# Optimization experiments

Hardware: AMD Instinct MI355X
Metric: run time of the kernel (lower is better)

Reference implementation:

```python
import jax, jax.numpy as jnp
import numpy as np

B, T, C = 4, 2048, 1024
H = 16
D = C // H  # head_dim = 64


def setup_inputs() -> dict:
    key = jax.random.key(0)
    k1, k2, k3 = jax.random.split(key, 3)
    x = jax.random.normal(k1, (B, T, C), dtype=jnp.float32)
    # torch Linear weights are [out_features, in_features]; scale like default init
    W_qkv = jax.random.normal(k2, (3 * C, C), dtype=jnp.float32) * (1.0 / np.sqrt(C))
    W_proj = jax.random.normal(k3, (C, C), dtype=jnp.float32) * (1.0 / np.sqrt(C))
    return {"x": x, "W_qkv": W_qkv, "W_proj": W_proj}


def reference(x, W_qkv, W_proj):
    # qkv projection: x @ W_qkv.T -> (B,T,3C), split into q,k,v
    qkv = jnp.einsum('btc,oc->bto', x, W_qkv)
    q, k, v = jnp.split(qkv, 3, axis=-1)
    # reshape to (B,H,T,D)
    q = q.reshape(B, T, H, D).transpose(0, 2, 1, 3)
    k = k.reshape(B, T, H, D).transpose(0, 2, 1, 3)
    v = v.reshape(B, T, H, D).transpose(0, 2, 1, 3)
    scale = jnp.sqrt(jnp.float32(D))
    # explicit (B,H,T,T) scores, as in the original module
    attn = jnp.einsum('bhqd,bhkd->bhqk', q, k) / scale
    causal = jnp.tril(jnp.ones((T, T), dtype=bool))
    attn = jnp.where(causal, attn, -jnp.inf)
    attn = jax.nn.softmax(attn, axis=-1)
    out = jnp.einsum('bhqk,bhkd->bhqd', attn, v)
    out = out.transpose(0, 2, 1, 3).reshape(B, T, C)
    return jnp.einsum('btc,oc->bto', out, W_proj)
```

## Files before the change

### kernel.cpp

```cpp
#include <hip/hip_runtime.h>

typedef __attribute__((ext_vector_type(8))) short short8;
typedef __attribute__((ext_vector_type(4))) float f32x4;
typedef __attribute__((ext_vector_type(16))) float f32x16;
typedef __attribute__((ext_vector_type(4))) unsigned int u32x4;

#define AS1(p) ((const __attribute__((address_space(1))) void*)(p))
#define AS3(p) ((__attribute__((address_space(3))) void*)(p))

#define B_ 4
#define T_ 2048
#define C_ 1024
#define H_ 16
#define D_ 64
#define M_ (B_*T_)

#define MFIX 16.0f

__device__ __forceinline__ unsigned short f2bf(float f) {
  union { float f; unsigned u; } v; v.f = f;
  return (unsigned short)((v.u + 0x7fffu + ((v.u >> 16) & 1u)) >> 16);
}

__device__ __forceinline__ unsigned cvt_pk_bf16(float lo, float hi2) {
  unsigned r;
  asm("v_cvt_pk_bf16_f32 %0, %1, %2" : "=v"(r) : "v"(lo), "v"(hi2));
  return r;
}

__device__ __forceinline__ float exp2_fast(float x) {
  return __builtin_amdgcn_exp2f(x);
}

__global__ void cast_f32_bf16(const float* __restrict__ in, unsigned short* __restrict__ out, int n) {
  int i = (blockIdx.x * blockDim.x + threadIdx.x) * 4;
  int stride = gridDim.x * blockDim.x * 4;
  for (; i < n; i += stride) {
    float4 f = *reinterpret_cast<const float4*>(in + i);
    ushort4 o;
    o.x = f2bf(f.x); o.y = f2bf(f.y); o.z = f2bf(f.z); o.w = f2bf(f.w);
    *reinterpret_cast<ushort4*>(out + i) = o;
  }
}

template<int EPI>
__global__ __launch_bounds__(256) void gemm_bt(
    const unsigned short* __restrict__ A, const unsigned short* __restrict__ Bt,
    float* __restrict__ Cout, int M, int N, int K,
    unsigned short* __restrict__ qb, unsigned short* __restrict__ kb,
    unsigned short* __restrict__ vtb) {
  __shared__ unsigned short As[2][128 * 32];
  __shared__ unsigned short Bs[2][128 * 32];
  const int tid = threadIdx.x;
  const int lane = tid & 63;
  const int w = tid >> 6;
  const int wr = w >> 1, wc = w & 1;
  const int lr = lane & 15, lg = lane >> 4;
  const int ntiles = N >> 7;
  const int nwg = gridDim.x;
  const int cpx = nwg >> 3;
  const int wg = (blockIdx.x & 7) * cpx + (blockIdx.x >> 3);
  const int mt = wg / ntiles, nt = wg % ntiles;
  const int m0 = mt << 7, n0 = nt << 7;

  f32x4 acc[4][4];
  #pragma unroll
  for (int i = 0; i < 4; i++)
    #pragma unroll
    for (int j = 0; j < 4; j++) acc[i][j] = (f32x4){0.f, 0.f, 0.f, 0.f};

  const int wbase = tid & ~63;

  auto stage = [&](int buf, int k0) {
    #pragma unroll
    for (int t = 0; t < 2; t++) {
      int slot = t * 256 + tid;
      int row = slot >> 2, kg = slot & 3;
      const unsigned short* ga = A + (size_t)(m0 + row) * K + k0 + kg * 8;
      char* la = (char*)As[buf] + (size_t)(t * 256 + wbase) * 16;
      __builtin_amdgcn_global_load_lds(AS1(ga), AS3(la), 16, 0, 0);
      const unsigned short* gb = Bt + (size_t)(n0 + row) * K + k0 + kg * 8;
      char* lb = (char*)Bs[buf] + (size_t)(t * 256 + wbase) * 16;
      __builtin_amdgcn_global_load_lds(AS1(gb), AS3(lb), 16, 0, 0);
    }
  };

  const int nIter = K >> 5;
  stage(0, 0);

  for (int it = 0; it < nIter; ++it) {
    const int cur = it & 1;
    if (it + 1 < nIter) {
      stage(cur ^ 1, (it + 1) << 5);
      asm volatile("s_waitcnt vmcnt(4)" ::: "memory");
    } else {
      asm volatile("s_waitcnt vmcnt(0)" ::: "memory");
    }
    __builtin_amdgcn_sched_barrier(0);
    __builtin_amdgcn_s_barrier();
    __builtin_amdgcn_sched_barrier(0);

    short8 af[4], bf[4];
    #pragma unroll
    for (int i = 0; i < 4; i++) {
      af[i] = *reinterpret_cast<const short8*>(&As[cur][(wr * 64 + i * 16 + lr) * 32 + lg * 8]);
      bf[i] = *reinterpret_cast<const short8*>(&Bs[cur][(wc * 64 + i * 16 + lr) * 32 + lg * 8]);
    }
    #pragma unroll
    for (int i = 0; i < 4; i++)
      #pragma unroll
      for (int j = 0; j < 4; j++)
        acc[i][j] = __builtin_amdgcn_mfma_f32_16x16x32_bf16(af[i], bf[j], acc[i][j], 0, 0, 0);

    __builtin_amdgcn_sched_barrier(0);
    __builtin_amdgcn_s_barrier();
  }

  #pragma unroll
  for (int i = 0; i < 4; i++) {
    #pragma unroll
    for (int j = 0; j < 4; j++) {
      #pragma unroll
      for (int r = 0; r < 4; r++) {
        int row = m0 + wr * 64 + i * 16 + lg * 4 + r;
        int col = n0 + wc * 64 + j * 16 + lr;
        float v = acc[i][j][r];
        if (EPI == 0) {
          Cout[(size_t)row * N + col] = v;
        } else {
          int which = col >> 10;
          int c = col & 1023;
          int h = c >> 6, d = c & 63;
          int b = row >> 11, t2 = row & 2047;
          if (which == 0) {
            qb[(((size_t)(b * H_ + h)) * T_ + t2) * D_ + d] = f2bf(v * 0.18033688f);
          } else if (which == 1) {
            kb[(((size_t)(b * H_ + h)) * T_ + t2) * D_ + d] = f2bf(v);
          } else {
            vtb[(((size_t)(b * H_ + h)) * D_ + d) * T_ + t2] = f2bf(v);
          }
        }
      }
    }
  }
}

__global__ __launch_bounds__(128, 2) void attn_fwd(
    const unsigned short* __restrict__ qb, const unsigned short* __restrict__ kb,
    const unsigned short* __restrict__ vtb, unsigned short* __restrict__ ob) {
  __shared__ unsigned short Kl[2 * 64 * 64];
  const int tid = threadIdx.x;
  const int lane = tid & 63;
  const int w = tid >> 6;
  const int q31 = lane & 31;
  const int hi = lane >> 5;

  const int bid = blockIdx.x;
  const int bh = (bid & 7) * 8 + ((bid >> 3) & 7);
  const int qt = 15 - (bid >> 6);
  const int qb0 = qt << 7;
  const int b = bh >> 4, h = bh & 15;

  const unsigned short* Q  = qb  + (size_t)bh * T_ * D_;
  const unsigned short* Kp = kb  + (size_t)bh * T_ * D_;
  const unsigned short* Vt = vtb + (size_t)bh * D_ * T_;

  const int qloA = qb0 + w * 64;
  const int qloB = qloA + 32;
  const int qgA = qloA + q31;
  const int qgB = qloB + q31;

  short8 qfA[4], qfB[4];
  #pragma unroll
  for (int ch = 0; ch < 4; ch++) {
    qfA[ch] = *reinterpret_cast<const short8*>(Q + qgA * D_ + ch * 16 + hi * 8);
    qfB[ch] = *reinterpret_cast<const short8*>(Q + qgB * D_ + ch * 16 + hi * 8);
  }

  f32x16 accA0, accA1, accB0, accB1;
  #pragma unroll
  for (int r = 0; r < 16; r++) { accA0[r] = 0.f; accA1[r] = 0.f; accB0[r] = 0.f; accB1[r] = 0.f; }
  float lA = 0.f, lB = 0.f;

  auto stage = [&](int buf, int k0) {
    #pragma unroll
    for (int sh = 0; sh < 4; sh++) {
      int s = sh * 128 + tid;
      int row = s >> 3;
      int xlin = (s & 7) * 16;
      int src = xlin ^ ((row & 7) << 4);
      const unsigned short* g = Kp + (k0 + row) * D_ + (src >> 1);
      char* l = (char*)Kl + buf * 8192 + (size_t)(sh * 128 + (tid & ~63)) * 16;
      __builtin_amdgcn_global_load_lds(AS1(g), AS3(l), 16, 0, 0);
    }
  };

  const int nt = qb0 / 64 + 2;
  stage(0, 0);
  __syncthreads();

  for (int t = 0; t < nt; t++) {
    const int k0 = t * 64;
    if (t + 1 < nt) stage((t + 1) & 1, k0 + 64);

    if (k0 <= qloA + 63) {
      short8 vf[2][4];
      #pragma unroll
      for (int ds = 0; ds < 2; ds++)
        #pragma unroll
        for (int kk = 0; kk < 4; kk++)
          vf[ds][kk] = *reinterpret_cast<const short8*>(
              Vt + (ds * 32 + q31) * T_ + k0 + kk * 16 + hi * 8);
      __builtin_amdgcn_sched_barrier(0);

      const char* kbase = (const char*)Kl + (t & 1) * 8192;

      f32x16 sA0, sA1, sB0, sB1;
      #pragma unroll
      for (int r = 0; r < 16; r++) { sA0[r] = 0.f; sA1[r] = 0.f; sB0[r] = 0.f; sB1[r] = 0.f; }
      __builtin_amdgcn_s_setprio(1);
      #pragma unroll
      for (int kc = 0; kc < 2; kc++) {
        const int row = kc * 32 + q31;
        const int sw = (row & 7) << 4;
        #pragma unroll
        for (int ch = 0; ch < 4; ch++) {
          short8 kf = *reinterpret_cast<const short8*>(kbase + row * 128 + ((ch * 32 + hi * 16) ^ sw));
          if (kc == 0) {
            sA0 = __builtin_amdgcn_mfma_f32_32x32x16_bf16(kf, qfA[ch], sA0, 0, 0, 0);
            sB0 = __builtin_amdgcn_mfma_f32_32x32x16_bf16(kf, qfB[ch], sB0, 0, 0, 0);
          } else {
            sA1 = __builtin_amdgcn_mfma_f32_32x32x16_bf16(kf, qfA[ch], sA1, 0, 0, 0);
            sB1 = __builtin_amdgcn_mfma_f32_32x32x16_bf16(kf, qfB[ch], sB1, 0, 0, 0);
          }
        }
      }
      __builtin_amdgcn_s_setprio(0);

      if (k0 + 63 > qloA) {
        #pragma unroll
        for (int r = 0; r < 16; r++) {
          const int kl = (r & 3) + 8 * (r >> 2) + 4 * hi;
          if (k0 + kl > qgA)      sA0[r] = -INFINITY;
          if (k0 + 32 + kl > qgA) sA1[r] = -INFINITY;
        }
      }
      if (k0 + 63 > qloB) {
        #pragma unroll
        for (int r = 0; r < 16; r++) {
          const int kl = (r & 3) + 8 * (r >> 2) + 4 * hi;
          if (k0 + kl > qgB)      sB0[r] = -INFINITY;
          if (k0 + 32 + kl > qgB) sB1[r] = -INFINITY;
        }
      }

      #pragma unroll
      for (int r = 0; r < 16; r++) {
        sA0[r] = exp2_fast(sA0[r] - MFIX); sA1[r] = exp2_fast(sA1[r] - MFIX);
        sB0[r] = exp2_fast(sB0[r] - MFIX); sB1[r] = exp2_fast(sB1[r] - MFIX);
      }
      {
        float tsA[8], tsB[8];
        #pragma unroll
        for (int r = 0; r < 8; r++) {
          tsA[r] = (sA0[r] + sA0[r + 8]) + (sA1[r] + sA1[r + 8]);
          tsB[r] = (sB0[r] + sB0[r + 8]) + (sB1[r] + sB1[r + 8]);
        }
        #pragma unroll
        for (int off = 4; off > 0; off >>= 1)
          #pragma unroll
          for (int r = 0; r < off; r++) { tsA[r] += tsA[r + off]; tsB[r] += tsB[r + off]; }
        lA += tsA[0];
        lB += tsB[0];
      }

      #pragma unroll
      for (int kc = 0; kc < 2; kc++) {
        unsigned w8A[8], rw8A[8], w8B[8], rw8B[8];
        #pragma unroll
        for (int j = 0; j < 8; j++) {
          float aA  = (kc == 0) ? sA0[2 * j] : sA1[2 * j];
          float bA  = (kc == 0) ? sA0[2 * j + 1] : sA1[2 * j + 1];
          w8A[j] = cvt_pk_bf16(aA, bA);
          float aB  = (kc == 0) ? sB0[2 * j] : sB1[2 * j];
          float bB  = (kc == 0) ? sB0[2 * j + 1] : sB1[2 * j + 1];
          w8B[j] = cvt_pk_bf16(aB, bB);
        }
        #pragma unroll
        for (int j = 0; j < 8; j++) {
          rw8A[j] = (unsigned)__shfl_xor((int)w8A[j], 32);
          rw8B[j] = (unsigned)__shfl_xor((int)w8B[j], 32);
        }

        __builtin_amdgcn_s_setprio(1);
        #pragma unroll
        for (int ks = 0; ks < 2; ks++) {
          unsigned a0 = hi ? rw8A[4 * ks + 2] : w8A[4 * ks + 0];
          unsigned a1 = hi ? rw8A[4 * ks + 3] : w8A[4 * ks + 1];
          unsigned a2 = hi ? w8A[4 * ks + 2]  : rw8A[4 * ks + 0];
          unsigned a3 = hi ? w8A[4 * ks + 3]  : rw8A[4 * ks + 1];
          u32x4 pwA = {a0, a1, a2, a3};
          unsigned b0 = hi ? rw8B[4 * ks + 2] : w8B[4 * ks + 0];
          unsigned b1 = hi ? rw8B[4 * ks + 3] : w8B[4 * ks + 1];
          unsigned b2 = hi ? w8B[4 * ks + 2]  : rw8B[4 * ks + 0];
          unsigned b3 = hi ? w8B[4 * ks + 3]  : rw8B[4 * ks + 1];
          u32x4 pwB = {b0, b1, b2, b3};
          union { u32x4 u; short8 s; } cvA, cvB;
          cvA.u = pwA; cvB.u = pwB;
          const int kk = kc * 2 + ks;
          #pragma unroll
          for (int ds = 0; ds < 2; ds++) {
            if (ds == 0) {
              accA0 = __builtin_amdgcn_mfma_f32_32x32x16_bf16(vf[0][kk], cvA.s, accA0, 0, 0, 0);
              accB0 = __builtin_amdgcn_mfma_f32_32x32x16_bf16(vf[0][kk], cvB.s, accB0, 0, 0, 0);
            } else {
              accA1 = __builtin_amdgcn_mfma_f32_32x32x16_bf16(vf[1][kk], cvA.s, accA1, 0, 0, 0);
              accB1 = __builtin_amdgcn_mfma_f32_32x32x16_bf16(vf[1][kk], cvB.s, accB1, 0, 0, 0);
            }
          }
        }
        __builtin_amdgcn_s_setprio(0);
      }
    }
    __syncthreads();
  }

  lA += __shfl_xor(lA, 32);
  lB += __shfl_xor(lB, 32);

  {
    const float invA = 1.f / lA;
    unsigned short* orow = ob + ((size_t)(b * T_ + qgA)) * C_ + h * D_;
    #pragma unroll
    for (int ds = 0; ds < 2; ds++) {
      #pragma unroll
      for (int g = 0; g < 4; g++) {
        ushort4 o4;
        if (ds == 0) {
          o4.x = f2bf(accA0[4 * g + 0] * invA); o4.y = f2bf(accA0[4 * g + 1] * invA);
          o4.z = f2bf(accA0[4 * g + 2] * invA); o4.w = f2bf(accA0[4 * g + 3] * invA);
        } else {
          o4.x = f2bf(accA1[4 * g + 0] * invA); o4.y = f2bf(accA1[4 * g + 1] * invA);
          o4.z = f2bf(accA1[4 * g + 2] * invA); o4.w = f2bf(accA1[4 * g + 3] * invA);
        }
        *reinterpret_cast<ushort4*>(orow + ds * 32 + 8 * g + 4 * hi) = o4;
      }
    }
  }
  {
    const float invB = 1.f / lB;
    unsigned short* orow = ob + ((size_t)(b * T_ + qgB)) * C_ + h * D_;
    #pragma unroll
    for (int ds = 0; ds < 2; ds++) {
      #pragma unroll
      for (int g = 0; g < 4; g++) {
        ushort4 o4;
        if (ds == 0) {
          o4.x = f2bf(accB0[4 * g + 0] * invB); o4.y = f2bf(accB0[4 * g + 1] * invB);
          o4.z = f2bf(accB0[4 * g + 2] * invB); o4.w = f2bf(accB0[4 * g + 3] * invB);
        } else {
          o4.x = f2bf(accB1[4 * g + 0] * invB); o4.y = f2bf(accB1[4 * g + 1] * invB);
          o4.z = f2bf(accB1[4 * g + 2] * invB); o4.w = f2bf(accB1[4 * g + 3] * invB);
        }
        *reinterpret_cast<ushort4*>(orow + ds * 32 + 8 * g + 4 * hi) = o4;
      }
    }
  }
}

extern "C" void kernel_launch(void* const* d_in, const int* in_sizes, int n_in,
                              void* d_out, int out_size, void* d_ws, size_t ws_size,
                              hipStream_t stream) {
  const float* x = (const float*)d_in[0];
  const float* W_qkv = (const float*)d_in[1];
  const float* W_proj = (const float*)d_in[2];
  float* out = (float*)d_out;

  char* ws = (char*)d_ws;
  unsigned short* xb     = (unsigned short*)(ws);
  unsigned short* wqkvb  = (unsigned short*)(ws + 16777216);
  unsigned short* wprojb = (unsigned short*)(ws + 23068672);
  unsigned short* qb     = (unsigned short*)(ws + 25165824);
  unsigned short* kb     = (unsigned short*)(ws + 41943040);
  unsigned short* vtb    = (unsigned short*)(ws + 58720256);
  unsigned short* ob     = xb;

  const int nx = M_ * C_;
  const int nwqkv = 3 * C_ * C_;
  const int nwproj = C_ * C_;

  cast_f32_bf16<<<2048, 256, 0, stream>>>(x, xb, nx);
  cast_f32_bf16<<<2048, 256, 0, stream>>>(W_qkv, wqkvb, nwqkv);
  cast_f32_bf16<<<1024, 256, 0, stream>>>(W_proj, wprojb, nwproj);

  gemm_bt<1><<<(M_ / 128) * (3 * C_ / 128), 256, 0, stream>>>(
      xb, wqkvb, nullptr, M_, 3 * C_, C_, qb, kb, vtb);

  attn_fwd<<<B_ * H_ * (T_ / 128), 128, 0, stream>>>(qb, kb, vtb, ob);

  gemm_bt<0><<<(M_ / 128) * (C_ / 128), 256, 0, stream>>>(
      ob, wprojb, out, M_, C_, C_, nullptr, nullptr, nullptr);
}
```

Baseline: 211.9 us.

## Add 256x256 swizzled-LDS QKV GEMM kernel and simplify projection GEMM sync

Replaces the 128x128 templated GEMM used for the QKV projection with a dedicated 512-thread kernel. It uses 256x256 output tiles, 64-wide K tiles, XOR-swizzled LDS staging, and a four-phase loop that issues the next tile's loads between MFMA groups, with raised wave priority during MFMAs. The goal is more data reuse per LDS load and fewer bank conflicts. The cost is 128 KB of LDS per block and a grid of only 384 blocks, which may leave CUs poorly balanced. The output-projection GEMM loses its template and now uses plain __syncthreads instead of hand-placed vmcnt waits and barriers.

```diff
diff --git a/kernel.cpp b/kernel.cpp
--- a/kernel.cpp
+++ b/kernel.cpp
@@ -43,12 +43,133 @@
   }
 }
 
-template<int EPI>
+__global__ __launch_bounds__(512, 2) void gemm256_qkv(
+    const unsigned short* __restrict__ A, const unsigned short* __restrict__ Bt,
+    int M, int N, int K,
+    unsigned short* __restrict__ qb, unsigned short* __restrict__ kb,
+    unsigned short* __restrict__ vtb) {
+  __shared__ unsigned short Ls[2][2][2][128 * 64];
+  const int tid = threadIdx.x;
+  const int lane = tid & 63;
+  const int wid = tid >> 6;
+  const int wm = wid >> 2;
+  const int wn = wid & 3;
+  const int lr = lane & 15, lg = lane >> 4;
+  const int ntb_cnt = N >> 8;
+  const int nwg = gridDim.x;
+  const int cpx = nwg >> 3;
+  const int wg = (blockIdx.x & 7) * cpx + (blockIdx.x >> 3);
+  const int mt = wg / ntb_cnt, ntb = wg % ntb_cnt;
+  const int m0 = mt << 8, n0 = ntb << 8;
+
+  f32x4 acc[8][4];
+  #pragma unroll
+  for (int i = 0; i < 8; i++)
+    #pragma unroll
+    for (int j = 0; j < 4; j++) acc[i][j] = (f32x4){0.f, 0.f, 0.f, 0.f};
+
+  const int wbase16 = (tid & ~63) * 16;
+
+  auto stage = [&](int buf, int mat, int half, int k0) {
+    const unsigned short* srcbase = (mat == 0) ? (A  + (size_t)(m0 + half * 128) * K)
+                                               : (Bt + (size_t)(n0 + half * 128) * K);
+    char* ldsbase = (char*)&Ls[buf][mat][half][0];
+    #pragma unroll
+    for (int i = 0; i < 2; i++) {
+      int s = i * 512 + tid;
+      int row = s >> 3;
+      int src = ((s & 7) * 16) ^ ((row & 7) << 4);
+      const unsigned short* g = srcbase + (size_t)row * K + k0 + (src >> 1);
+      char* l = ldsbase + i * 8192 + wbase16;
+      __builtin_amdgcn_global_load_lds(AS1(g), AS3(l), 16, 0, 0);
+    }
+  };
+
+  const int ktiles = K >> 6;
+  stage(0, 0, 0, 0); stage(0, 0, 1, 0); stage(0, 1, 0, 0); stage(0, 1, 1, 0);
+
+  for (int t = 0; t < ktiles; ++t) {
+    const int cur = t & 1;
+    const int nk0 = (t + 1) << 6;
+    const bool more = (t + 1 < ktiles);
+    short8 bfrag[4][2];
+
+    #pragma unroll
+    for (int p = 0; p < 4; p++) {
+      if (more) stage(cur ^ 1, p >> 1, p & 1, nk0);
+      if (p == 0) {
+        if (more) asm volatile("s_waitcnt vmcnt(2)" ::: "memory");
+        else      asm volatile("s_waitcnt vmcnt(0)" ::: "memory");
+      }
+      __builtin_amdgcn_sched_barrier(0);
+      __builtin_amdgcn_s_barrier();
+      __builtin_amdgcn_sched_barrier(0);
+
+      if (p == 0) {
+        #pragma unroll
+        for (int ni = 0; ni < 4; ni++)
+          #pragma unroll
+          for (int ks = 0; ks < 2; ks++) {
+            const int rih = (wn & 1) * 64 + ni * 16 + lr;
+            bfrag[ni][ks] = *reinterpret_cast<const short8*>(
+                (const char*)&Ls[cur][1][wn >> 1][0] + rih * 128 +
+                ((ks * 64 + lg * 16) ^ ((lr & 7) << 4)));
+          }
+      }
+      short8 af[2][2];
+      #pragma unroll
+      for (int m2 = 0; m2 < 2; m2++)
+        #pragma unroll
+        for (int ks = 0; ks < 2; ks++) {
+          const int rih = (2 * p + m2) * 16 + lr;
+          af[m2][ks] = *reinterpret_cast<const short8*>(
+              (const char*)&Ls[cur][0][wm][0] + rih * 128 +
+              ((ks * 64 + lg * 16) ^ ((lr & 7) << 4)));
+        }
+
+      __builtin_amdgcn_s_setprio(1);
+      #pragma unroll
+      for (int m2 = 0; m2 < 2; m2++)
+        #pragma unroll
+        for (int ni = 0; ni < 4; ni++)
+          #pragma unroll
+          for (int ks = 0; ks < 2; ks++)
+            acc[2 * p + m2][ni] = __builtin_amdgcn_mfma_f32_16x16x32_bf16(
+                af[m2][ks], bfrag[ni][ks], acc[2 * p + m2][ni], 0, 0, 0);
+      __builtin_amdgcn_s_setprio(0);
+      __builtin_amdgcn_sched_barrier(0);
+      __builtin_amdgcn_s_barrier();
+    }
+  }
+
+  #pragma unroll
+  for (int mi = 0; mi < 8; mi++) {
+    #pragma unroll
+    for (int ni = 0; ni < 4; ni++) {
+      #pragma unroll
+      for (int r = 0; r < 4; r++) {
+        int row = m0 + wm * 128 + mi * 16 + lg * 4 + r;
+        int col = n0 + wn * 64 + ni * 16 + lr;
+        float v = acc[mi][ni][r];
+        int which = col >> 10;
+        int c = col & 1023;
+        int h = c >> 6, d = c & 63;
+        int b = row >> 11, t2 = row & 2047;
+        if (which == 0) {
+          qb[(((size_t)(b * H_ + h)) * T_ + t2) * D_ + d] = f2bf(v * 0.18033688f);
+        } else if (which == 1) {
+          kb[(((size_t)(b * H_ + h)) * T_ + t2) * D_ + d] = f2bf(v);
+        } else {
+          vtb[(((size_t)(b * H_ + h)) * D_ + d) * T_ + t2] = f2bf(v);
+        }
+      }
+    }
+  }
+}
+
 __global__ __launch_bounds__(256) void gemm_bt(
     const unsigned short* __restrict__ A, const unsigned short* __restrict__ Bt,
-    float* __restrict__ Cout, int M, int N, int K,
-    unsigned short* __restrict__ qb, unsigned short* __restrict__ kb,
-    unsigned short* __restrict__ vtb) {
+    float* __restrict__ Cout, int M, int N, int K) {
   __shared__ unsigned short As[2][128 * 32];
   __shared__ unsigned short Bs[2][128 * 32];
   const int tid = threadIdx.x;
@@ -87,18 +208,11 @@
 
   const int nIter = K >> 5;
   stage(0, 0);
+  __syncthreads();
 
   for (int it = 0; it < nIter; ++it) {
     const int cur = it & 1;
-    if (it + 1 < nIter) {
-      stage(cur ^ 1, (it + 1) << 5);
-      asm volatile("s_waitcnt vmcnt(4)" ::: "memory");
-    } else {
-      asm volatile("s_waitcnt vmcnt(0)" ::: "memory");
-    }
-    __builtin_amdgcn_sched_barrier(0);
-    __builtin_amdgcn_s_barrier();
-    __builtin_amdgcn_sched_barrier(0);
+    if (it + 1 < nIter) stage(cur ^ 1, (it + 1) << 5);
 
     short8 af[4], bf[4];
     #pragma unroll
@@ -112,37 +226,19 @@
       for (int j = 0; j < 4; j++)
         acc[i][j] = __builtin_amdgcn_mfma_f32_16x16x32_bf16(af[i], bf[j], acc[i][j], 0, 0, 0);
 
-    __builtin_amdgcn_sched_barrier(0);
-    __builtin_amdgcn_s_barrier();
-  }
-
-  #pragma unroll
-  for (int i = 0; i < 4; i++) {
-    #pragma unroll
-    for (int j = 0; j < 4; j++) {
+    __syncthreads();
+  }
+
+  #pragma unroll
+  for (int i = 0; i < 4; i++)
+    #pragma unroll
+    for (int j = 0; j < 4; j++)
       #pragma unroll
       for (int r = 0; r < 4; r++) {
         int row = m0 + wr * 64 + i * 16 + lg * 4 + r;
         int col = n0 + wc * 64 + j * 16 + lr;
-        float v = acc[i][j][r];
-        if (EPI == 0) {
-          Cout[(size_t)row * N + col] = v;
-        } else {
-          int which = col >> 10;
-          int c = col & 1023;
-          int h = c >> 6, d = c & 63;
-          int b = row >> 11, t2 = row & 2047;
-          if (which == 0) {
-            qb[(((size_t)(b * H_ + h)) * T_ + t2) * D_ + d] = f2bf(v * 0.18033688f);
-          } else if (which == 1) {
-            kb[(((size_t)(b * H_ + h)) * T_ + t2) * D_ + d] = f2bf(v);
-          } else {
-            vtb[(((size_t)(b * H_ + h)) * D_ + d) * T_ + t2] = f2bf(v);
-          }
-        }
-      }
-    }
-  }
+        Cout[(size_t)row * N + col] = acc[i][j][r];
+      }
 }
 
 __global__ __launch_bounds__(128, 2) void attn_fwd(
@@ -393,11 +489,11 @@
   cast_f32_bf16<<<2048, 256, 0, stream>>>(W_qkv, wqkvb, nwqkv);
   cast_f32_bf16<<<1024, 256, 0, stream>>>(W_proj, wprojb, nwproj);
 
-  gemm_bt<1><<<(M_ / 128) * (3 * C_ / 128), 256, 0, stream>>>(
-      xb, wqkvb, nullptr, M_, 3 * C_, C_, qb, kb, vtb);
+  gemm256_qkv<<<(M_ / 256) * (3 * C_ / 256), 512, 0, stream>>>(
+      xb, wqkvb, M_, 3 * C_, C_, qb, kb, vtb);
 
   attn_fwd<<<B_ * H_ * (T_ / 128), 128, 0, stream>>>(qb, kb, vtb, ob);
 
-  gemm_bt<0><<<(M_ / 128) * (C_ / 128), 256, 0, stream>>>(
-      ob, wprojb, out, M_, C_, C_, nullptr, nullptr, nullptr);
-}
+  gemm_bt<<<(M_ / 128) * (C_ / 128), 256, 0, stream>>>(
+      ob, wprojb, out, M_, C_, C_);
+}
```

New measurement: 205.2 us. -3.2%, faster.

## Split attention into single-wave 64-query blocks and simplify GEMM pipeline sync

Applied to the files above, without the earlier changes.

The attention kernel now launches one 64-lane wave per block covering 64 queries, instead of two waves covering 128. That removes the per-tile __syncthreads and the idle causal tiles the second wave used to skip. K staging is driven by explicit vmcnt waits within the single wave, and the causal mask runs only on the final diagonal tile. The QKV and output GEMM loops replace the hand-tuned vmcnt(4) wait plus s_barrier with a plain __syncthreads. This may serialise the prefetch of the next K-slice with the current compute, and it depends on the compiler inserting a wait for the LDS-DMA loads.

```diff
diff --git a/kernel.cpp b/kernel.cpp
--- a/kernel.cpp
+++ b/kernel.cpp
@@ -87,18 +87,11 @@
 
   const int nIter = K >> 5;
   stage(0, 0);
+  __syncthreads();
 
   for (int it = 0; it < nIter; ++it) {
     const int cur = it & 1;
-    if (it + 1 < nIter) {
-      stage(cur ^ 1, (it + 1) << 5);
-      asm volatile("s_waitcnt vmcnt(4)" ::: "memory");
-    } else {
-      asm volatile("s_waitcnt vmcnt(0)" ::: "memory");
-    }
-    __builtin_amdgcn_sched_barrier(0);
-    __builtin_amdgcn_s_barrier();
-    __builtin_amdgcn_sched_barrier(0);
+    if (it + 1 < nIter) stage(cur ^ 1, (it + 1) << 5);
 
     short8 af[4], bf[4];
     #pragma unroll
@@ -112,8 +105,7 @@
       for (int j = 0; j < 4; j++)
         acc[i][j] = __builtin_amdgcn_mfma_f32_16x16x32_bf16(af[i], bf[j], acc[i][j], 0, 0, 0);
 
-    __builtin_amdgcn_sched_barrier(0);
-    __builtin_amdgcn_s_barrier();
+    __syncthreads();
   }
 
   #pragma unroll
@@ -145,28 +137,26 @@
   }
 }
 
-__global__ __launch_bounds__(128, 2) void attn_fwd(
+__global__ __launch_bounds__(64, 3) void attn_fwd(
     const unsigned short* __restrict__ qb, const unsigned short* __restrict__ kb,
     const unsigned short* __restrict__ vtb, unsigned short* __restrict__ ob) {
   __shared__ unsigned short Kl[2 * 64 * 64];
-  const int tid = threadIdx.x;
-  const int lane = tid & 63;
-  const int w = tid >> 6;
+  const int lane = threadIdx.x;
   const int q31 = lane & 31;
   const int hi = lane >> 5;
 
   const int bid = blockIdx.x;
   const int bh = (bid & 7) * 8 + ((bid >> 3) & 7);
-  const int qt = 15 - (bid >> 6);
-  const int qb0 = qt << 7;
+  const int qt = 31 - (bid >> 6);
+  const int qb0 = qt << 6;
   const int b = bh >> 4, h = bh & 15;
 
   const unsigned short* Q  = qb  + (size_t)bh * T_ * D_;
   const unsigned short* Kp = kb  + (size_t)bh * T_ * D_;
   const unsigned short* Vt = vtb + (size_t)bh * D_ * T_;
 
-  const int qloA = qb0 + w * 64;
-  const int qloB = qloA + 32;
+  const int qloA = qb0;
+  const int qloB = qb0 + 32;
   const int qgA = qloA + q31;
   const int qgB = qloB + q31;
 
@@ -184,145 +174,140 @@
 
   auto stage = [&](int buf, int k0) {
     #pragma unroll
-    for (int sh = 0; sh < 4; sh++) {
-      int s = sh * 128 + tid;
+    for (int sh = 0; sh < 8; sh++) {
+      int s = sh * 64 + lane;
       int row = s >> 3;
-      int xlin = (s & 7) * 16;
-      int src = xlin ^ ((row & 7) << 4);
+      int src = ((s & 7) * 16) ^ ((row & 7) << 4);
       const unsigned short* g = Kp + (k0 + row) * D_ + (src >> 1);
-      char* l = (char*)Kl + buf * 8192 + (size_t)(sh * 128 + (tid & ~63)) * 16;
+      char* l = (char*)Kl + buf * 8192 + sh * 1024;
       __builtin_amdgcn_global_load_lds(AS1(g), AS3(l), 16, 0, 0);
     }
   };
 
-  const int nt = qb0 / 64 + 2;
+  const int nt = qt + 1;
   stage(0, 0);
-  __syncthreads();
 
   for (int t = 0; t < nt; t++) {
     const int k0 = t * 64;
-    if (t + 1 < nt) stage((t + 1) & 1, k0 + 64);
-
-    if (k0 <= qloA + 63) {
-      short8 vf[2][4];
-      #pragma unroll
-      for (int ds = 0; ds < 2; ds++)
+    if (t + 1 < nt) {
+      stage((t + 1) & 1, k0 + 64);
+      asm volatile("s_waitcnt vmcnt(8)" ::: "memory");
+    } else {
+      asm volatile("s_waitcnt vmcnt(0)" ::: "memory");
+    }
+    __builtin_amdgcn_sched_barrier(0);
+
+    short8 vf[2][4];
+    #pragma unroll
+    for (int ds = 0; ds < 2; ds++)
+      #pragma unroll
+      for (int kk = 0; kk < 4; kk++)
+        vf[ds][kk] = *reinterpret_cast<const short8*>(
+            Vt + (ds * 32 + q31) * T_ + k0 + kk * 16 + hi * 8);
+    __builtin_amdgcn_sched_barrier(0);
+
+    const char* kbase = (const char*)Kl + (t & 1) * 8192;
+
+    f32x16 sA0, sA1, sB0, sB1;
+    #pragma unroll
+    for (int r = 0; r < 16; r++) { sA0[r] = 0.f; sA1[r] = 0.f; sB0[r] = 0.f; sB1[r] = 0.f; }
+    __builtin_amdgcn_s_setprio(1);
+    #pragma unroll
+    for (int kc = 0; kc < 2; kc++) {
+      const int row = kc * 32 + q31;
+      const int sw = (row & 7) << 4;
+      #pragma unroll
+      for (int ch = 0; ch < 4; ch++) {
+        short8 kf = *reinterpret_cast<const short8*>(kbase + row * 128 + ((ch * 32 + hi * 16) ^ sw));
+        if (kc == 0) {
+          sA0 = __builtin_amdgcn_mfma_f32_32x32x16_bf16(kf, qfA[ch], sA0, 0, 0, 0);
+          sB0 = __builtin_amdgcn_mfma_f32_32x32x16_bf16(kf, qfB[ch], sB0, 0, 0, 0);
+        } else {
+          sA1 = __builtin_amdgcn_mfma_f32_32x32x16_bf16(kf, qfA[ch], sA1, 0, 0, 0);
+          sB1 = __builtin_amdgcn_mfma_f32_32x32x16_bf16(kf, qfB[ch], sB1, 0, 0, 0);
+        }
+      }
+    }
+    __builtin_amdgcn_s_setprio(0);
+
+    if (t == nt - 1) {
+      #pragma unroll
+      for (int r = 0; r < 16; r++) {
+        const int kl = (r & 3) + 8 * (r >> 2) + 4 * hi;
+        if (k0 + kl > qgA)      sA0[r] = -INFINITY;
+        if (k0 + 32 + kl > qgA) sA1[r] = -INFINITY;
+        if (k0 + kl > qgB)      sB0[r] = -INFINITY;
+        if (k0 + 32 + kl > qgB) sB1[r] = -INFINITY;
+      }
+    }
+
+    #pragma unroll
+    for (int r = 0; r < 16; r++) {
+      sA0[r] = exp2_fast(sA0[r] - MFIX); sA1[r] = exp2_fast(sA1[r] - MFIX);
+      sB0[r] = exp2_fast(sB0[r] - MFIX); sB1[r] = exp2_fast(sB1[r] - MFIX);
+    }
+    {
+      float tsA[8], tsB[8];
+      #pragma unroll
+      for (int r = 0; r < 8; r++) {
+        tsA[r] = (sA0[r] + sA0[r + 8]) + (sA1[r] + sA1[r + 8]);
+        tsB[r] = (sB0[r] + sB0[r + 8]) + (sB1[r] + sB1[r + 8]);
+      }
+      #pragma unroll
+      for (int off = 4; off > 0; off >>= 1)
         #pragma unroll
-        for (int kk = 0; kk < 4; kk++)
-          vf[ds][kk] = *reinterpret_cast<const short8*>(
-              Vt + (ds * 32 + q31) * T_ + k0 + kk * 16 + hi * 8);
-      __builtin_amdgcn_sched_barrier(0);
-
-      const char* kbase = (const char*)Kl + (t & 1) * 8192;
-
-      f32x16 sA0, sA1, sB0, sB1;
-      #pragma unroll
-      for (int r = 0; r < 16; r++) { sA0[r] = 0.f; sA1[r] = 0.f; sB0[r] = 0.f; sB1[r] = 0.f; }
+        for (int r = 0; r < off; r++) { tsA[r] += tsA[r + off]; tsB[r] += tsB[r + off]; }
+      lA += tsA[0];
+      lB += tsB[0];
+    }
+
+    #pragma unroll
+    for (int kc = 0; kc < 2; kc++) {
+      unsigned w8A[8], rw8A[8], w8B[8], rw8B[8];
+      #pragma unroll
+      for (int j = 0; j < 8; j++) {
+        float aA  = (kc == 0) ? sA0[2 * j] : sA1[2 * j];
+        float bA  = (kc == 0) ? sA0[2 * j + 1] : sA1[2 * j + 1];
+        w8A[j] = cvt_pk_bf16(aA, bA);
+        float aB  = (kc == 0) ? sB0[2 * j] : sB1[2 * j];
+        float bB  = (kc == 0) ? sB0[2 * j + 1] : sB1[2 * j + 1];
+        w8B[j] = cvt_pk_bf16(aB, bB);
+      }
+      #pragma unroll
+      for (int j = 0; j < 8; j++) {
+        rw8A[j] = (unsigned)__shfl_xor((int)w8A[j], 32);
+        rw8B[j] = (unsigned)__shfl_xor((int)w8B[j], 32);
+      }
+
       __builtin_amdgcn_s_setprio(1);
       #pragma unroll
-      for (int kc = 0; kc < 2; kc++) {
-        const int row = kc * 32 + q31;
-        const int sw = (row & 7) << 4;
+      for (int ks = 0; ks < 2; ks++) {
+        unsigned a0 = hi ? rw8A[4 * ks + 2] : w8A[4 * ks + 0];
+        unsigned a1 = hi ? rw8A[4 * ks + 3] : w8A[4 * ks + 1];
+        unsigned a2 = hi ? w8A[4 * ks + 2]  : rw8A[4 * ks + 0];
+        unsigned a3 = hi ? w8A[4 * ks + 3]  : rw8A[4 * ks + 1];
+        u32x4 pwA = {a0, a1, a2, a3};
+        unsigned b0 = hi ? rw8B[4 * ks + 2] : w8B[4 * ks + 0];
+        unsigned b1 = hi ? rw8B[4 * ks + 3] : w8B[4 * ks + 1];
+        unsigned b2 = hi ? w8B[4 * ks + 2]  : rw8B[4 * ks + 0];
+        unsigned b3 = hi ? w8B[4 * ks + 3]  : rw8B[4 * ks + 1];
+        u32x4 pwB = {b0, b1, b2, b3};
+        union { u32x4 u; short8 s; } cvA, cvB;
+        cvA.u = pwA; cvB.u = pwB;
+        const int kk = kc * 2 + ks;
         #pragma unroll
-        for (int ch = 0; ch < 4; ch++) {
-          short8 kf = *reinterpret_cast<const short8*>(kbase + row * 128 + ((ch * 32 + hi * 16) ^ sw));
-          if (kc == 0) {
-            sA0 = __builtin_amdgcn_mfma_f32_32x32x16_bf16(kf, qfA[ch], sA0, 0, 0, 0);
-            sB0 = __builtin_amdgcn_mfma_f32_32x32x16_bf16(kf, qfB[ch], sB0, 0, 0, 0);
+        for (int ds = 0; ds < 2; ds++) {
+          if (ds == 0) {
+            accA0 = __builtin_amdgcn_mfma_f32_32x32x16_bf16(vf[0][kk], cvA.s, accA0, 0, 0, 0);
+            accB0 = __builtin_amdgcn_mfma_f32_32x32x16_bf16(vf[0][kk], cvB.s, accB0, 0, 0, 0);
           } else {
-            sA1 = __builtin_amdgcn_mfma_f32_32x32x16_bf16(kf, qfA[ch], sA1, 0, 0, 0);
-            sB1 = __builtin_amdgcn_mfma_f32_32x32x16_bf16(kf, qfB[ch], sB1, 0, 0, 0);
+            accA1 = __builtin_amdgcn_mfma_f32_32x32x16_bf16(vf[1][kk], cvA.s, accA1, 0, 0, 0);
+            accB1 = __builtin_amdgcn_mfma_f32_32x32x16_bf16(vf[1][kk], cvB.s, accB1, 0, 0, 0);
           }
         }
       }
       __builtin_amdgcn_s_setprio(0);
-
-      if (k0 + 63 > qloA) {
-        #pragma unroll
-        for (int r = 0; r < 16; r++) {
-          const int kl = (r & 3) + 8 * (r >> 2) + 4 * hi;
-          if (k0 + kl > qgA)      sA0[r] = -INFINITY;
-          if (k0 + 32 + kl > qgA) sA1[r] = -INFINITY;
-        }
-      }
-      if (k0 + 63 > qloB) {
-        #pragma unroll
-        for (int r = 0; r < 16; r++) {
-          const int kl = (r & 3) + 8 * (r >> 2) + 4 * hi;
-          if (k0 + kl > qgB)      sB0[r] = -INFINITY;
-          if (k0 + 32 + kl > qgB) sB1[r] = -INFINITY;
-        }
-      }
-
-      #pragma unroll
-      for (int r = 0; r < 16; r++) {
-        sA0[r] = exp2_fast(sA0[r] - MFIX); sA1[r] = exp2_fast(sA1[r] - MFIX);
-        sB0[r] = exp2_fast(sB0[r] - MFIX); sB1[r] = exp2_fast(sB1[r] - MFIX);
-      }
-      {
-        float tsA[8], tsB[8];
-        #pragma unroll
-        for (int r = 0; r < 8; r++) {
-          tsA[r] = (sA0[r] + sA0[r + 8]) + (sA1[r] + sA1[r + 8]);
-          tsB[r] = (sB0[r] + sB0[r + 8]) + (sB1[r] + sB1[r + 8]);
-        }
-        #pragma unroll
-        for (int off = 4; off > 0; off >>= 1)
-          #pragma unroll
-          for (int r = 0; r < off; r++) { tsA[r] += tsA[r + off]; tsB[r] += tsB[r + off]; }
-        lA += tsA[0];
-        lB += tsB[0];
-      }
-
-      #pragma unroll
-      for (int kc = 0; kc < 2; kc++) {
-        unsigned w8A[8], rw8A[8], w8B[8], rw8B[8];
-        #pragma unroll
-        for (int j = 0; j < 8; j++) {
-          float aA  = (kc == 0) ? sA0[2 * j] : sA1[2 * j];
-          float bA  = (kc == 0) ? sA0[2 * j + 1] : sA1[2 * j + 1];
-          w8A[j] = cvt_pk_bf16(aA, bA);
-          float aB  = (kc == 0) ? sB0[2 * j] : sB1[2 * j];
-          float bB  = (kc == 0) ? sB0[2 * j + 1] : sB1[2 * j + 1];
-          w8B[j] = cvt_pk_bf16(aB, bB);
-        }
-        #pragma unroll
-        for (int j = 0; j < 8; j++) {
-          rw8A[j] = (unsigned)__shfl_xor((int)w8A[j], 32);
-          rw8B[j] = (unsigned)__shfl_xor((int)w8B[j], 32);
-        }
-
-        __builtin_amdgcn_s_setprio(1);
-        #pragma unroll
-        for (int ks = 0; ks < 2; ks++) {
-          unsigned a0 = hi ? rw8A[4 * ks + 2] : w8A[4 * ks + 0];
-          unsigned a1 = hi ? rw8A[4 * ks + 3] : w8A[4 * ks + 1];
-          unsigned a2 = hi ? w8A[4 * ks + 2]  : rw8A[4 * ks + 0];
-          unsigned a3 = hi ? w8A[4 * ks + 3]  : rw8A[4 * ks + 1];
-          u32x4 pwA = {a0, a1, a2, a3};
-          unsigned b0 = hi ? rw8B[4 * ks + 2] : w8B[4 * ks + 0];
-          unsigned b1 = hi ? rw8B[4 * ks + 3] : w8B[4 * ks + 1];
-          unsigned b2 = hi ? w8B[4 * ks + 2]  : rw8B[4 * ks + 0];
-          unsigned b3 = hi ? w8B[4 * ks + 3]  : rw8B[4 * ks + 1];
-          u32x4 pwB = {b0, b1, b2, b3};
-          union { u32x4 u; short8 s; } cvA, cvB;
-          cvA.u = pwA; cvB.u = pwB;
-          const int kk = kc * 2 + ks;
-          #pragma unroll
-          for (int ds = 0; ds < 2; ds++) {
-            if (ds == 0) {
-              accA0 = __builtin_amdgcn_mfma_f32_32x32x16_bf16(vf[0][kk], cvA.s, accA0, 0, 0, 0);
-              accB0 = __builtin_amdgcn_mfma_f32_32x32x16_bf16(vf[0][kk], cvB.s, accB0, 0, 0, 0);
-            } else {
-              accA1 = __builtin_amdgcn_mfma_f32_32x32x16_bf16(vf[1][kk], cvA.s, accA1, 0, 0, 0);
-              accB1 = __builtin_amdgcn_mfma_f32_32x32x16_bf16(vf[1][kk], cvB.s, accB1, 0, 0, 0);
-            }
-          }
-        }
-        __builtin_amdgcn_s_setprio(0);
-      }
-    }
-    __syncthreads();
+    }
   }
 
   lA += __shfl_xor(lA, 32);
@@ -396,7 +381,7 @@
   gemm_bt<1><<<(M_ / 128) * (3 * C_ / 128), 256, 0, stream>>>(
       xb, wqkvb, nullptr, M_, 3 * C_, C_, qb, kb, vtb);
 
-  attn_fwd<<<B_ * H_ * (T_ / 128), 128, 0, stream>>>(qb, kb, vtb, ob);
+  attn_fwd<<<B_ * H_ * (T_ / 64), 64, 0, stream>>>(qb, kb, vtb, ob);
 
   gemm_bt<0><<<(M_ / 128) * (C_ / 128), 256, 0, stream>>>(
       ob, wprojb, out, M_, C_, C_, nullptr, nullptr, nullptr);
```

After: 387.4 us. 82.8% more time.
